# Performance work log

Measured on AMD Instinct MI355X. Metric: run time of the kernel, lower is better.

The kernel has to match this reference:

```python
import jax, jax.numpy as jnp
import numpy as np


def _mlp(x, w1, b1, w2, b2):
    # generic 2-layer MLP (stand-in for ConfiguredModule's combine_mlp / embedding_mlp)
    return jax.nn.gelu(x @ w1 + b1) @ w2 + b2


def setup_inputs() -> dict:
    key = jax.random.key(0)
    ks = jax.random.split(key, 8)
    B, N, A = 8, 128, 64          # molecules, atoms, nfeature
    Rr, Ra = 32, 16               # radial / angular geometry shifts
    P = N * (N - 1) // 2          # 8128 atom pairs
    d_pair, H, nembed = 32, 512, 256

    def rnd(k, shp, scale=1.0):
        return jax.random.normal(k, shp, dtype=jnp.float32) * scale

    return {
        "gr": rnd(ks[0], (B, N, Rr, N), 0.1),
        "ga": rnd(ks[1], (B, N, Ra, P), 0.1),
        "afv": rnd(ks[2], (B, N, A)),
        # combine_mlp: 2A -> 2A -> d_pair
        "cw1": rnd(ks[3], (2 * A, 2 * A), 1.0 / np.sqrt(2 * A)),
        "cb1": jnp.zeros((2 * A,), jnp.float32),
        "cw2": rnd(ks[4], (2 * A, d_pair), 1.0 / np.sqrt(2 * A)),
        "cb2": jnp.zeros((d_pair,), jnp.float32),
        # embedding_mlp: Rr*A + Ra*d_pair -> H -> nembed
        "ew1": rnd(ks[5], (Rr * A + Ra * d_pair, H), 1.0 / np.sqrt(Rr * A + Ra * d_pair)),
        "eb1": jnp.zeros((H,), jnp.float32),
        "ew2": rnd(ks[6], (H, nembed), 1.0 / np.sqrt(H)),
        "eb2": jnp.zeros((nembed,), jnp.float32),
    }


def reference(gr, ga, afv, cw1, cb1, cw2, cb2, ew1, eb1, ew2, eb2):
    B, N, A = afv.shape
    # _combine_afv_1: pairwise outer sum/product, upper-triangular (i<j) pairs.
    # Instead of materializing [B, 2A, N, N] and masking, gather pairs directly
    # (row-major i<j order matches torch's triu boolean-mask indexing).
    ii, jj = jnp.triu_indices(N, k=1)           # [P]
    ai = afv[:, ii, :]                           # [B, P, A]
    aj = afv[:, jj, :]                           # [B, P, A]
    afv_pair = jnp.concatenate([ai + aj, ai * aj], axis=-1)  # [B, P, 2A]
    afv_pair = _mlp(afv_pair, cw1, cb1, cw2, cb2)            # [B, P, d_pair]

    # grv = matmul(gr, afv[:, None]) : [B, N, Rr, N] @ [B, 1, N, A] -> [B, N, Rr, A]
    grv = jnp.einsum('bnrm,bma->bnra', gr, afv).reshape(B, N, -1)
    # gav = matmul(ga, afv_pair[:, None]) : [B, N, Ra, P] @ [B, 1, P, d] -> [B, N, Ra, d]
    gav = jnp.einsum('bnap,bpd->bnad', ga, afv_pair).reshape(B, N, -1)

    aef = _mlp(jnp.concatenate([grv, gav], axis=-1), ew1, eb1, ew2, eb2)  # [B, N, nembed]
    return aef, afv
```

## Files before the change

### kernel.cpp

```cpp
#include <hip/hip_runtime.h>
#include <math.h>

#define BB 8
#define NN 128
#define AA 64
#define RR 32
#define RA 16
#define PP 8128
#define DP 32
#define HH 512
#define EE 256
#define XDIM 2560

static constexpr size_t WS_PAIRT = 0;
static constexpr size_t WS_XB    = WS_PAIRT + (size_t)BB*DP*PP/2;
static constexpr size_t WS_EW1B  = WS_XB + (size_t)BB*NN*XDIM/2;
static constexpr size_t WS_CW1T  = WS_EW1B + (size_t)HH*XDIM/2;
static constexpr size_t WS_CW2T  = WS_CW1T + (size_t)128*128/2;
static constexpr size_t WS_EW2B  = WS_CW2T + (size_t)DP*128/2;
static constexpr size_t WS_HB    = WS_EW2B + (size_t)EE*HH/2;

typedef __attribute__((ext_vector_type(8))) short bf16x8;
typedef __attribute__((ext_vector_type(4))) float f32x4;

__device__ __forceinline__ float gelu_f(float x) {
    float u = 0.7978845608028654f * (x + 0.044715f * x * x * x);
    float au = fabsf(u);
    float e = __expf(-2.0f * au);
    float th = (1.0f - e) / (1.0f + e);
    th = copysignf(th, u);
    return 0.5f * x * (1.0f + th);
}

__device__ __forceinline__ unsigned short f2bf(float x) {
    union { float f; unsigned u; } v; v.f = x;
    unsigned r = v.u + 0x7fffu + ((v.u >> 16) & 1u);
    return (unsigned short)(r >> 16);
}

__device__ __forceinline__ bf16x8 pack_bf16x8(float4 a, float4 b) {
    bf16x8 r;
    r[0] = (short)f2bf(a.x); r[1] = (short)f2bf(a.y);
    r[2] = (short)f2bf(a.z); r[3] = (short)f2bf(a.w);
    r[4] = (short)f2bf(b.x); r[5] = (short)f2bf(b.y);
    r[6] = (short)f2bf(b.z); r[7] = (short)f2bf(b.w);
    return r;
}

__global__ __launch_bounds__(256) void prep_k(
    const float* __restrict__ cw1, const float* __restrict__ cw2,
    unsigned short* __restrict__ cw1T, unsigned short* __restrict__ cw2T)
{
    const int bid = blockIdx.x, t = threadIdx.x;
    if (bid < 16) {
        int idx = bid * 256 + t;
        int n = idx >> 5;
        int k0 = (idx & 31) * 4;
        ushort4 o;
        o.x = f2bf(cw1[(size_t)(k0 + 0) * 128 + n]);
        o.y = f2bf(cw1[(size_t)(k0 + 1) * 128 + n]);
        o.z = f2bf(cw1[(size_t)(k0 + 2) * 128 + n]);
        o.w = f2bf(cw1[(size_t)(k0 + 3) * 128 + n]);
        *(ushort4*)(cw1T + (size_t)n * 128 + k0) = o;
    } else {
        int idx = (bid - 16) * 256 + t;
        int d = idx >> 5;
        int k0 = (idx & 31) * 4;
        ushort4 o;
        o.x = f2bf(cw2[(size_t)(k0 + 0) * DP + d]);
        o.y = f2bf(cw2[(size_t)(k0 + 1) * DP + d]);
        o.z = f2bf(cw2[(size_t)(k0 + 2) * DP + d]);
        o.w = f2bf(cw2[(size_t)(k0 + 3) * DP + d]);
        *(ushort4*)(cw2T + (size_t)d * 128 + k0) = o;
    }
}

__global__ __launch_bounds__(256) void stage1_k(
    const float* __restrict__ afv, const unsigned short* __restrict__ cw1T,
    const float* __restrict__ cb1, const unsigned short* __restrict__ cw2T,
    const float* __restrict__ cb2, unsigned short* __restrict__ pairT)
{
    __shared__ unsigned short sm[16384];
    __shared__ int iis[64], jjs[64];
    const int bid = blockIdx.x;
    const int t = threadIdx.x;
    const int w = t >> 6, lane = t & 63;
    const int lm = lane & 15, lg = lane >> 4;

    const int b = bid / 127;
    const int pbase = (bid % 127) * 64;
    unsigned short* X = sm;
    unsigned short* Hs = sm + 8192;

    if (t < 64) {
        int p = pbase + t;
        int i = 0;
        while (i < 126) {
            int nx = i + 1;
            int off = nx * 127 - (nx * (nx - 1)) / 2;
            if (off <= p) i = nx; else break;
        }
        int off = i * 127 - (i * (i - 1)) / 2;
        iis[t] = i;
        jjs[t] = i + 1 + (p - off);
    }
    __syncthreads();
    {
        int pp = t & 63, seg = t >> 6;
        const float* ar = afv + (size_t)(b * NN + iis[pp]) * AA + seg * 16;
        const float* br = afv + (size_t)(b * NN + jjs[pp]) * AA + seg * 16;
        float4 xa = *(const float4*)(ar),     xb2 = *(const float4*)(ar + 4);
        float4 xc = *(const float4*)(ar + 8), xd = *(const float4*)(ar + 12);
        float4 ya = *(const float4*)(br),     yb = *(const float4*)(br + 4);
        float4 yc = *(const float4*)(br + 8), yd = *(const float4*)(br + 12);
        float4 s0 = make_float4(xa.x + ya.x, xa.y + ya.y, xa.z + ya.z, xa.w + ya.w);
        float4 s1 = make_float4(xb2.x + yb.x, xb2.y + yb.y, xb2.z + yb.z, xb2.w + yb.w);
        float4 s2 = make_float4(xc.x + yc.x, xc.y + yc.y, xc.z + yc.z, xc.w + yc.w);
        float4 s3 = make_float4(xd.x + yd.x, xd.y + yd.y, xd.z + yd.z, xd.w + yd.w);
        float4 p0 = make_float4(xa.x * ya.x, xa.y * ya.y, xa.z * ya.z, xa.w * ya.w);
        float4 p1 = make_float4(xb2.x * yb.x, xb2.y * yb.y, xb2.z * yb.z, xb2.w * yb.w);
        float4 p2 = make_float4(xc.x * yc.x, xc.y * yc.y, xc.z * yc.z, xc.w * yc.w);
        float4 p3 = make_float4(xd.x * yd.x, xd.y * yd.y, xd.z * yd.z, xd.w * yd.w);
        int gs = seg * 2, gp = 8 + seg * 2, sw = pp & 7;
        *(bf16x8*)(X + pp * 128 + (((gs + 0) ^ sw) * 8)) = pack_bf16x8(s0, s1);
        *(bf16x8*)(X + pp * 128 + (((gs + 1) ^ sw) * 8)) = pack_bf16x8(s2, s3);
        *(bf16x8*)(X + pp * 128 + (((gp + 0) ^ sw) * 8)) = pack_bf16x8(p0, p1);
        *(bf16x8*)(X + pp * 128 + (((gp + 1) ^ sw) * 8)) = pack_bf16x8(p2, p3);
    }
    __syncthreads();
    const int wn = w * 32;
    f32x4 acc1[4][2];
    #pragma unroll
    for (int i = 0; i < 4; ++i)
        #pragma unroll
        for (int j = 0; j < 2; ++j) acc1[i][j] = 0.f;
    #pragma unroll
    for (int ks = 0; ks < 4; ++ks) {
        int g = ks * 4 + lg;
        bf16x8 a[4];
        #pragma unroll
        for (int mi = 0; mi < 4; ++mi) {
            int row = mi * 16 + lm;
            a[mi] = *(const bf16x8*)(X + row * 128 + ((g ^ (row & 7)) * 8));
        }
        #pragma unroll
        for (int ni = 0; ni < 2; ++ni) {
            bf16x8 bv = *(const bf16x8*)(cw1T + (size_t)(wn + ni * 16 + lm) * 128 +
                                         ks * 32 + lg * 8);
            #pragma unroll
            for (int mi = 0; mi < 4; ++mi)
                acc1[mi][ni] = __builtin_amdgcn_mfma_f32_16x16x32_bf16(
                    a[mi], bv, acc1[mi][ni], 0, 0, 0);
        }
    }
    #pragma unroll
    for (int ni = 0; ni < 2; ++ni) {
        int n = wn + ni * 16 + lm;
        float bb = cb1[n];
        int gn = n >> 3, ne = n & 7;
        #pragma unroll
        for (int mi = 0; mi < 4; ++mi)
            #pragma unroll
            for (int r = 0; r < 4; ++r) {
                int row = mi * 16 + lg * 4 + r;
                Hs[row * 128 + ((gn ^ (row & 7)) * 8 + ne)] =
                    f2bf(gelu_f(acc1[mi][ni][r] + bb));
            }
    }
    __syncthreads();
    f32x4 acc2[2];
    acc2[0] = 0.f; acc2[1] = 0.f;
    #pragma unroll
    for (int ks = 0; ks < 4; ++ks) {
        int row = w * 16 + lm;
        int g = ks * 4 + lg;
        bf16x8 a2 = *(const bf16x8*)(Hs + row * 128 + ((g ^ (row & 7)) * 8));
        #pragma unroll
        for (int ni = 0; ni < 2; ++ni) {
            bf16x8 bv = *(const bf16x8*)(cw2T + (size_t)(ni * 16 + lm) * 128 +
                                         ks * 32 + lg * 8);
            acc2[ni] = __builtin_amdgcn_mfma_f32_16x16x32_bf16(a2, bv, acc2[ni], 0, 0, 0);
        }
    }
    {
        unsigned short* T = sm;
        __syncthreads();
        #pragma unroll
        for (int ni = 0; ni < 2; ++ni) {
            int d = ni * 16 + lm;
            float bb = cb2[d];
            #pragma unroll
            for (int r = 0; r < 4; ++r) {
                int p = w * 16 + lg * 4 + r;
                T[d * 64 + p] = f2bf(acc2[ni][r] + bb);
            }
        }
        __syncthreads();
        int d = t >> 3, slot = t & 7;
        bf16x8 v = *(const bf16x8*)(T + d * 64 + slot * 8);
        *(bf16x8*)(pairT + ((size_t)b * DP + d) * PP + pbase + slot * 8) = v;
    }
}

__global__ __launch_bounds__(256) void gav_k(
    const float* __restrict__ ga, const unsigned short* __restrict__ pairT,
    unsigned short* __restrict__ Xb,
    const float* __restrict__ gr, const float* __restrict__ afv,
    const float* __restrict__ ew1, unsigned short* __restrict__ ew1bT,
    const float* __restrict__ ew2, unsigned short* __restrict__ ew2bT,
    float* __restrict__ out2)
{
    __shared__ unsigned short sm[24576];
    const int bid = blockIdx.x;
    const int t = threadIdx.x;
    const int w = t >> 6, lane = t & 63;
    const int lm = lane & 15, lg = lane >> 4;

    if (bid >= 2176) {
        int idx = (bid - 2176) * 256 + t;
        float4 v = *(const float4*)(afv + (size_t)idx * 4);
        *(float4*)(out2 + (size_t)idx * 4) = v;
        return;
    }
    if (bid >= 2048) {
        int q = (bid - 2048) * 256 + t;
        int n = q & 255;
        int k0 = (q >> 8) * 4;
        ushort4 o;
        o.x = f2bf(ew2[(size_t)(k0 + 0) * EE + n]);
        o.y = f2bf(ew2[(size_t)(k0 + 1) * EE + n]);
        o.z = f2bf(ew2[(size_t)(k0 + 2) * EE + n]);
        o.w = f2bf(ew2[(size_t)(k0 + 3) * EE + n]);
        *(ushort4*)(ew2bT + (size_t)n * HH + k0) = o;
        return;
    }
    if (bid >= 768) {
        int q = (bid - 768) * 256 + t;
        int n = q & 511;
        int k0 = (q >> 9) * 4;
        ushort4 o;
        o.x = f2bf(ew1[(size_t)(k0 + 0) * HH + n]);
        o.y = f2bf(ew1[(size_t)(k0 + 1) * HH + n]);
        o.z = f2bf(ew1[(size_t)(k0 + 2) * HH + n]);
        o.w = f2bf(ew1[(size_t)(k0 + 3) * HH + n]);
        *(ushort4*)(ew1bT + (size_t)n * XDIM + k0) = o;
        return;
    }

    if (bid >= 512) {
        const int gb = bid - 512;
        const int b = gb >> 5;
        const int rbase = (gb & 31) * 128;
        const float* gab = gr + ((size_t)b * 4096 + rbase) * NN;
        unsigned short* As  = sm;
        unsigned short* Bs2 = sm + 16384;
        {
            const int srow = t >> 1, half = t & 1;
            const float* arow = gab + (size_t)srow * NN + half * 64;
            #pragma unroll
            for (int q = 0; q < 8; ++q) {
                float4 x0 = *(const float4*)(arow + q * 8);
                float4 x1 = *(const float4*)(arow + q * 8 + 4);
                bf16x8 v = pack_bf16x8(x0, x1);
                int g = half * 8 + q;
                *(bf16x8*)(As + srow * 128 + ((g ^ (srow & 7)) * 8)) = v;
            }
        }
        #pragma unroll
        for (int q = 0; q < 8; ++q) {
            int pos = t + q * 256;
            int m = pos >> 4, f4i = pos & 15;
            float4 v = *(const float4*)(afv + (size_t)(b * NN + m) * AA + f4i * 4);
            int gm = m >> 3, me = m & 7;
            float vv[4] = {v.x, v.y, v.z, v.w};
            #pragma unroll
            for (int i = 0; i < 4; ++i) {
                int a = f4i * 4 + i;
                Bs2[a * 128 + ((gm ^ (a & 7)) * 8 + me)] = f2bf(vv[i]);
            }
        }
        __syncthreads();
        const int wm = w * 32;
        f32x4 acc[2][4];
        #pragma unroll
        for (int i = 0; i < 2; ++i)
            #pragma unroll
            for (int j = 0; j < 4; ++j) acc[i][j] = 0.f;
        #pragma unroll
        for (int ks = 0; ks < 4; ++ks) {
            int g = ks * 4 + lg;
            int r0 = wm + lm, r1 = wm + 16 + lm;
            bf16x8 a0 = *(const bf16x8*)(As + r0 * 128 + ((g ^ (r0 & 7)) * 8));
            bf16x8 a1 = *(const bf16x8*)(As + r1 * 128 + ((g ^ (r1 & 7)) * 8));
            #pragma unroll
            for (int ni = 0; ni < 4; ++ni) {
                int a = ni * 16 + lm;
                bf16x8 bv = *(const bf16x8*)(Bs2 + a * 128 + ((g ^ (a & 7)) * 8));
                acc[0][ni] = __builtin_amdgcn_mfma_f32_16x16x32_bf16(a0, bv, acc[0][ni], 0, 0, 0);
                acc[1][ni] = __builtin_amdgcn_mfma_f32_16x16x32_bf16(a1, bv, acc[1][ni], 0, 0, 0);
            }
        }
        __syncthreads();
        unsigned short* T = sm;
        #pragma unroll
        for (int mi = 0; mi < 2; ++mi)
            #pragma unroll
            for (int ni = 0; ni < 4; ++ni)
                #pragma unroll
                for (int r = 0; r < 4; ++r)
                    T[(wm + mi * 16 + lg * 4 + r) * 64 + ni * 16 + lm] =
                        f2bf(acc[mi][ni][r]);
        __syncthreads();
        #pragma unroll
        for (int q = 0; q < 4; ++q) {
            int idx = t + q * 256;
            int rr2 = idx >> 3, slot = idx & 7;
            bf16x8 v = *(const bf16x8*)(T + rr2 * 64 + slot * 8);
            int grow = rbase + rr2;
            *(bf16x8*)(Xb + ((size_t)(b * NN) + (grow >> 5)) * XDIM +
                       (grow & 31) * 64 + slot * 8) = v;
        }
        return;
    }

    const int b = bid & 7, rt = bid >> 3;
    const int rbase = rt * 32;
    const int srow = t >> 3, slot = t & 7;
    const int wr = (w & 1) * 16, wc = (w >> 1) * 16;
    unsigned short* As = sm;
    unsigned short* Bs = sm + 4096;

    f32x4 acc = 0.f;

    const float* gab = ga + (size_t)(b * 2048 + rbase) * PP;
    const unsigned short* pbT = pairT + (size_t)b * DP * PP;

    float4 ra[4];
    bf16x8 rb0, rb1;
    {
        int k0 = slot * 8;
        ra[0] = *(const float4*)(gab + (size_t)srow * PP + k0);
        ra[1] = *(const float4*)(gab + (size_t)srow * PP + k0 + 4);
        ra[2] = *(const float4*)(gab + (size_t)srow * PP + k0 + 64);
        ra[3] = *(const float4*)(gab + (size_t)srow * PP + k0 + 68);
        rb0 = *(const bf16x8*)(pbT + (size_t)srow * PP + k0);
        rb1 = *(const bf16x8*)(pbT + (size_t)srow * PP + k0 + 64);
    }

    for (int it = 0; it < 64; ++it) {
        __syncthreads();
        const int sw = srow & 7;
        const int g0 = (slot ^ sw) * 8;
        const int g1 = ((slot ^ sw) + 8) * 8;
        *(bf16x8*)(As + srow * 128 + g0) = pack_bf16x8(ra[0], ra[1]);
        *(bf16x8*)(As + srow * 128 + g1) = pack_bf16x8(ra[2], ra[3]);
        *(bf16x8*)(Bs + srow * 128 + g0) = rb0;
        *(bf16x8*)(Bs + srow * 128 + g1) = rb1;
        __syncthreads();
        if (it + 1 < 64) {
            int kn = (it + 1) * 128 + slot * 8;
            int k1 = kn + 64; if (k1 > PP - 8) k1 = PP - 8;
            ra[0] = *(const float4*)(gab + (size_t)srow * PP + kn);
            ra[1] = *(const float4*)(gab + (size_t)srow * PP + kn + 4);
            ra[2] = *(const float4*)(gab + (size_t)srow * PP + k1);
            ra[3] = *(const float4*)(gab + (size_t)srow * PP + k1 + 4);
            rb0 = *(const bf16x8*)(pbT + (size_t)srow * PP + kn);
            rb1 = *(const bf16x8*)(pbT + (size_t)srow * PP + k1);
        }
        if (it < 63) {
            #pragma unroll
            for (int ks = 0; ks < 4; ++ks) {
                int gg = ks * 4 + lg;
                int rowa = wr + lm;
                int rowb = wc + lm;
                bf16x8 a  = *(const bf16x8*)(As + rowa * 128 + ((gg ^ (rowa & 7)) * 8));
                bf16x8 bv = *(const bf16x8*)(Bs + rowb * 128 + ((gg ^ (rowb & 7)) * 8));
                acc = __builtin_amdgcn_mfma_f32_16x16x32_bf16(a, bv, acc, 0, 0, 0);
            }
        } else {
            #pragma unroll
            for (int ks = 0; ks < 2; ++ks) {
                int gg = ks * 4 + lg;
                int rowa = wr + lm;
                int rowb = wc + lm;
                bf16x8 a  = *(const bf16x8*)(As + rowa * 128 + ((gg ^ (rowa & 7)) * 8));
                bf16x8 bv = *(const bf16x8*)(Bs + rowb * 128 + ((gg ^ (rowb & 7)) * 8));
                acc = __builtin_amdgcn_mfma_f32_16x16x32_bf16(a, bv, acc, 0, 0, 0);
            }
        }
    }
    #pragma unroll
    for (int r = 0; r < 4; ++r) {
        int grow = rbase + wr + lg * 4 + r;
        int n = grow >> 4, a2 = grow & 15;
        int d = wc + lm;
        Xb[(size_t)(b * NN + n) * XDIM + 2048 + a2 * DP + d] = f2bf(acc[r]);
    }
}

__global__ __launch_bounds__(256) void mlp1_k(
    const unsigned short* __restrict__ Xb,
    const unsigned short* __restrict__ Wt,
    const float* __restrict__ eb1, unsigned short* __restrict__ Hb)
{
    __shared__ unsigned short As[32 * 64];
    __shared__ unsigned short Bs[32 * 64];
    const int bid = blockIdx.x;
    const int ct = bid & 15, rt = bid >> 4;
    const int rbase = rt * 32, nbase = ct * 32;
    const int t = threadIdx.x;
    const int w = t >> 6, lane = t & 63;
    const int lm = lane & 15, lg = lane >> 4;
    const int wr = (w & 1) * 16, wc = (w >> 1) * 16;
    const int srow = t >> 3, sg = t & 7;

    f32x4 acc = 0.f;

    const unsigned short* Arow = Xb + (size_t)(rbase + srow) * XDIM;
    const unsigned short* Brow = Wt + (size_t)(nbase + srow) * XDIM;

    bf16x8 rA = *(const bf16x8*)(Arow + sg * 8);
    bf16x8 rB = *(const bf16x8*)(Brow + sg * 8);

    for (int it = 0; it < 40; ++it) {
        __syncthreads();
        const int sw = srow & 7;
        *(bf16x8*)(As + srow * 64 + ((sg ^ sw) * 8)) = rA;
        *(bf16x8*)(Bs + srow * 64 + ((sg ^ sw) * 8)) = rB;
        __syncthreads();
        if (it + 1 < 40) {
            int kn = (it + 1) * 64;
            rA = *(const bf16x8*)(Arow + kn + sg * 8);
            rB = *(const bf16x8*)(Brow + kn + sg * 8);
        }
        #pragma unroll
        for (int ks = 0; ks < 2; ++ks) {
            int g = ks * 4 + lg;
            int r0 = wr + lm, r1 = wc + lm;
            bf16x8 a  = *(const bf16x8*)(As + r0 * 64 + ((g ^ (r0 & 7)) * 8));
            bf16x8 bv = *(const bf16x8*)(Bs + r1 * 64 + ((g ^ (r1 & 7)) * 8));
            acc = __builtin_amdgcn_mfma_f32_16x16x32_bf16(a, bv, acc, 0, 0, 0);
        }
    }
    const int col = nbase + wc + lm;
    const float bb = eb1[col];
    #pragma unroll
    for (int r = 0; r < 4; ++r) {
        int row = rbase + wr + lg * 4 + r;
        Hb[(size_t)row * HH + col] = f2bf(gelu_f(acc[r] + bb));
    }
}

__global__ __launch_bounds__(256) void mlp2_k(
    const unsigned short* __restrict__ Hb,
    const unsigned short* __restrict__ Wt,
    const float* __restrict__ eb2, float* __restrict__ out)
{
    __shared__ unsigned short As[32 * 64];
    __shared__ unsigned short Bs[32 * 64];
    const int bid = blockIdx.x;
    const int ct = bid & 7, rt = bid >> 3;
    const int rbase = rt * 32, nbase = ct * 32;
    const int t = threadIdx.x;
    const int w = t >> 6, lane = t & 63;
    const int lm = lane & 15, lg = lane >> 4;
    const int wr = (w & 1) * 16, wc = (w >> 1) * 16;
    const int srow = t >> 3, sg = t & 7;

    f32x4 acc = 0.f;

    const unsigned short* Arow = Hb + (size_t)(rbase + srow) * HH;
    const unsigned short* Brow = Wt + (size_t)(nbase + srow) * HH;

    bf16x8 rA = *(const bf16x8*)(Arow + sg * 8);
    bf16x8 rB = *(const bf16x8*)(Brow + sg * 8);

    for (int it = 0; it < 8; ++it) {
        __syncthreads();
        const int sw = srow & 7;
        *(bf16x8*)(As + srow * 64 + ((sg ^ sw) * 8)) = rA;
        *(bf16x8*)(Bs + srow * 64 + ((sg ^ sw) * 8)) = rB;
        __syncthreads();
        if (it + 1 < 8) {
            int kn = (it + 1) * 64;
            rA = *(const bf16x8*)(Arow + kn + sg * 8);
            rB = *(const bf16x8*)(Brow + kn + sg * 8);
        }
        #pragma unroll
        for (int ks = 0; ks < 2; ++ks) {
            int g = ks * 4 + lg;
            int r0 = wr + lm, r1 = wc + lm;
            bf16x8 a  = *(const bf16x8*)(As + r0 * 64 + ((g ^ (r0 & 7)) * 8));
            bf16x8 bv = *(const bf16x8*)(Bs + r1 * 64 + ((g ^ (r1 & 7)) * 8));
            acc = __builtin_amdgcn_mfma_f32_16x16x32_bf16(a, bv, acc, 0, 0, 0);
        }
    }
    const int col = nbase + wc + lm;
    const float bb = eb2[col];
    #pragma unroll
    for (int r = 0; r < 4; ++r) {
        int row = rbase + wr + lg * 4 + r;
        out[(size_t)row * EE + col] = acc[r] + bb;
    }
}

extern "C" void kernel_launch(void* const* d_in, const int* in_sizes, int n_in,
                              void* d_out, int out_size, void* d_ws, size_t ws_size,
                              hipStream_t stream) {
    const float* gr  = (const float*)d_in[0];
    const float* ga  = (const float*)d_in[1];
    const float* afv = (const float*)d_in[2];
    const float* cw1 = (const float*)d_in[3];
    const float* cb1 = (const float*)d_in[4];
    const float* cw2 = (const float*)d_in[5];
    const float* cb2 = (const float*)d_in[6];
    const float* ew1 = (const float*)d_in[7];
    const float* eb1 = (const float*)d_in[8];
    const float* ew2 = (const float*)d_in[9];
    const float* eb2 = (const float*)d_in[10];
    float* out = (float*)d_out;
    float* ws = (float*)d_ws;

    unsigned short* pairT  = (unsigned short*)(ws + WS_PAIRT);
    unsigned short* Xb     = (unsigned short*)(ws + WS_XB);
    unsigned short* ew1bT  = (unsigned short*)(ws + WS_EW1B);
    unsigned short* cw1T   = (unsigned short*)(ws + WS_CW1T);
    unsigned short* cw2T   = (unsigned short*)(ws + WS_CW2T);
    unsigned short* ew2bT  = (unsigned short*)(ws + WS_EW2B);
    unsigned short* Hb     = (unsigned short*)(ws + WS_HB);

    prep_k<<<dim3(20), dim3(256), 0, stream>>>(cw1, cw2, cw1T, cw2T);
    stage1_k<<<dim3(1016), dim3(256), 0, stream>>>(afv, cw1T, cb1, cw2T, cb2, pairT);
    gav_k<<<dim3(2240), dim3(256), 0, stream>>>(ga, pairT, Xb, gr, afv,
                                                ew1, ew1bT, ew2, ew2bT,
                                                out + (size_t)BB * NN * EE);
    mlp1_k<<<dim3(512), dim3(256), 0, stream>>>(Xb, ew1bT, eb1, Hb);
    mlp2_k<<<dim3(256), dim3(256), 0, stream>>>(Hb, ew2bT, eb2, out);
}
```

Baseline: 180.7 us.

## Double-buffer LDS tiles in GEMM kernels and remap blocks across XCDs

```diff
diff --git a/kernel.cpp b/kernel.cpp
--- a/kernel.cpp
+++ b/kernel.cpp
@@ -327,8 +327,6 @@
     const int rbase = rt * 32;
     const int srow = t >> 3, slot = t & 7;
     const int wr = (w & 1) * 16, wc = (w >> 1) * 16;
-    unsigned short* As = sm;
-    unsigned short* Bs = sm + 4096;
 
     f32x4 acc = 0.f;
 
@@ -337,44 +335,51 @@
 
     float4 ra[4];
     bf16x8 rb0, rb1;
-    {
-        int k0 = slot * 8;
-        ra[0] = *(const float4*)(gab + (size_t)srow * PP + k0);
-        ra[1] = *(const float4*)(gab + (size_t)srow * PP + k0 + 4);
-        ra[2] = *(const float4*)(gab + (size_t)srow * PP + k0 + 64);
-        ra[3] = *(const float4*)(gab + (size_t)srow * PP + k0 + 68);
-        rb0 = *(const bf16x8*)(pbT + (size_t)srow * PP + k0);
-        rb1 = *(const bf16x8*)(pbT + (size_t)srow * PP + k0 + 64);
-    }
+
+#define GAV_LOAD(IT)                                                         \
+    {                                                                        \
+        int kn = (IT) * 128 + slot * 8;                                      \
+        int k1 = kn + 64; if (k1 > PP - 8) k1 = PP - 8;                      \
+        ra[0] = *(const float4*)(gab + (size_t)srow * PP + kn);              \
+        ra[1] = *(const float4*)(gab + (size_t)srow * PP + kn + 4);          \
+        ra[2] = *(const float4*)(gab + (size_t)srow * PP + k1);              \
+        ra[3] = *(const float4*)(gab + (size_t)srow * PP + k1 + 4);          \
+        rb0 = *(const bf16x8*)(pbT + (size_t)srow * PP + kn);                \
+        rb1 = *(const bf16x8*)(pbT + (size_t)srow * PP + k1);                \
+    }
+
+#define GAV_WRITE(BUF)                                                      \
+    {                                                                        \
+        unsigned short* A_ = sm + (BUF) * 8192;                              \
+        unsigned short* B_ = A_ + 4096;                                      \
+        const int sw_ = srow & 7;                                            \
+        const int g0_ = (slot ^ sw_) * 8;                                    \
+        const int g1_ = ((slot ^ sw_) + 8) * 8;                              \
+        *(bf16x8*)(A_ + srow * 128 + g0_) = pack_bf16x8(ra[0], ra[1]);       \
+        *(bf16x8*)(A_ + srow * 128 + g1_) = pack_bf16x8(ra[2], ra[3]);       \
+        *(bf16x8*)(B_ + srow * 128 + g0_) = rb0;                             \
+        *(bf16x8*)(B_ + srow * 128 + g1_) = rb1;                             \
+    }
+
+    GAV_LOAD(0);
+    GAV_WRITE(0);
+    __syncthreads();
+    GAV_LOAD(1);
 
     for (int it = 0; it < 64; ++it) {
-        __syncthreads();
-        const int sw = srow & 7;
-        const int g0 = (slot ^ sw) * 8;
-        const int g1 = ((slot ^ sw) + 8) * 8;
-        *(bf16x8*)(As + srow * 128 + g0) = pack_bf16x8(ra[0], ra[1]);
-        *(bf16x8*)(As + srow * 128 + g1) = pack_bf16x8(ra[2], ra[3]);
-        *(bf16x8*)(Bs + srow * 128 + g0) = rb0;
-        *(bf16x8*)(Bs + srow * 128 + g1) = rb1;
-        __syncthreads();
-        if (it + 1 < 64) {
-            int kn = (it + 1) * 128 + slot * 8;
-            int k1 = kn + 64; if (k1 > PP - 8) k1 = PP - 8;
-            ra[0] = *(const float4*)(gab + (size_t)srow * PP + kn);
-            ra[1] = *(const float4*)(gab + (size_t)srow * PP + kn + 4);
-            ra[2] = *(const float4*)(gab + (size_t)srow * PP + k1);
-            ra[3] = *(const float4*)(gab + (size_t)srow * PP + k1 + 4);
-            rb0 = *(const bf16x8*)(pbT + (size_t)srow * PP + kn);
-            rb1 = *(const bf16x8*)(pbT + (size_t)srow * PP + k1);
-        }
+        const int cur = it & 1;
+        const unsigned short* Ac = sm + cur * 8192;
+        const unsigned short* Bc = Ac + 4096;
+        if (it + 1 < 64) GAV_WRITE(cur ^ 1);
+        if (it + 2 < 64) GAV_LOAD(it + 2);
         if (it < 63) {
             #pragma unroll
             for (int ks = 0; ks < 4; ++ks) {
                 int gg = ks * 4 + lg;
                 int rowa = wr + lm;
                 int rowb = wc + lm;
-                bf16x8 a  = *(const bf16x8*)(As + rowa * 128 + ((gg ^ (rowa & 7)) * 8));
-                bf16x8 bv = *(const bf16x8*)(Bs + rowb * 128 + ((gg ^ (rowb & 7)) * 8));
+                bf16x8 a  = *(const bf16x8*)(Ac + rowa * 128 + ((gg ^ (rowa & 7)) * 8));
+                bf16x8 bv = *(const bf16x8*)(Bc + rowb * 128 + ((gg ^ (rowb & 7)) * 8));
                 acc = __builtin_amdgcn_mfma_f32_16x16x32_bf16(a, bv, acc, 0, 0, 0);
             }
         } else {
@@ -383,11 +388,12 @@
                 int gg = ks * 4 + lg;
                 int rowa = wr + lm;
                 int rowb = wc + lm;
-                bf16x8 a  = *(const bf16x8*)(As + rowa * 128 + ((gg ^ (rowa & 7)) * 8));
-                bf16x8 bv = *(const bf16x8*)(Bs + rowb * 128 + ((gg ^ (rowb & 7)) * 8));
+                bf16x8 a  = *(const bf16x8*)(Ac + rowa * 128 + ((gg ^ (rowa & 7)) * 8));
+                bf16x8 bv = *(const bf16x8*)(Bc + rowb * 128 + ((gg ^ (rowb & 7)) * 8));
                 acc = __builtin_amdgcn_mfma_f32_16x16x32_bf16(a, bv, acc, 0, 0, 0);
             }
         }
+        __syncthreads();
     }
     #pragma unroll
     for (int r = 0; r < 4; ++r) {
@@ -403,10 +409,11 @@
     const unsigned short* __restrict__ Wt,
     const float* __restrict__ eb1, unsigned short* __restrict__ Hb)
 {
-    __shared__ unsigned short As[32 * 64];
-    __shared__ unsigned short Bs[32 * 64];
+    __shared__ unsigned short sm[8192];
     const int bid = blockIdx.x;
-    const int ct = bid & 15, rt = bid >> 4;
+    const int xcd = bid & 7, idx = bid >> 3;
+    const int rt = (xcd << 2) | (idx & 3);
+    const int ct = idx >> 2;
     const int rbase = rt * 32, nbase = ct * 32;
     const int t = threadIdx.x;
     const int w = t >> 6, lane = t & 63;
@@ -419,28 +426,35 @@
     const unsigned short* Arow = Xb + (size_t)(rbase + srow) * XDIM;
     const unsigned short* Brow = Wt + (size_t)(nbase + srow) * XDIM;
 
-    bf16x8 rA = *(const bf16x8*)(Arow + sg * 8);
-    bf16x8 rB = *(const bf16x8*)(Brow + sg * 8);
+    bf16x8 rA, rB;
+
+#define M1_LOAD(IT)  { rA = *(const bf16x8*)(Arow + (IT) * 64 + sg * 8);     \
+                       rB = *(const bf16x8*)(Brow + (IT) * 64 + sg * 8); }
+#define M1_WRITE(BUF) { unsigned short* A_ = sm + (BUF) * 4096;              \
+                        unsigned short* B_ = A_ + 2048;                      \
+                        const int sw_ = srow & 7;                            \
+                        *(bf16x8*)(A_ + srow * 64 + ((sg ^ sw_) * 8)) = rA;  \
+                        *(bf16x8*)(B_ + srow * 64 + ((sg ^ sw_) * 8)) = rB; }
+
+    M1_LOAD(0); M1_WRITE(0);
+    __syncthreads();
+    M1_LOAD(1);
 
     for (int it = 0; it < 40; ++it) {
-        __syncthreads();
-        const int sw = srow & 7;
-        *(bf16x8*)(As + srow * 64 + ((sg ^ sw) * 8)) = rA;
-        *(bf16x8*)(Bs + srow * 64 + ((sg ^ sw) * 8)) = rB;
-        __syncthreads();
-        if (it + 1 < 40) {
-            int kn = (it + 1) * 64;
-            rA = *(const bf16x8*)(Arow + kn + sg * 8);
-            rB = *(const bf16x8*)(Brow + kn + sg * 8);
-        }
+        const int cur = it & 1;
+        const unsigned short* Ac = sm + cur * 4096;
+        const unsigned short* Bc = Ac + 2048;
+        if (it + 1 < 40) M1_WRITE(cur ^ 1);
+        if (it + 2 < 40) M1_LOAD(it + 2);
         #pragma unroll
         for (int ks = 0; ks < 2; ++ks) {
             int g = ks * 4 + lg;
             int r0 = wr + lm, r1 = wc + lm;
-            bf16x8 a  = *(const bf16x8*)(As + r0 * 64 + ((g ^ (r0 & 7)) * 8));
-            bf16x8 bv = *(const bf16x8*)(Bs + r1 * 64 + ((g ^ (r1 & 7)) * 8));
+            bf16x8 a  = *(const bf16x8*)(Ac + r0 * 64 + ((g ^ (r0 & 7)) * 8));
+            bf16x8 bv = *(const bf16x8*)(Bc + r1 * 64 + ((g ^ (r1 & 7)) * 8));
             acc = __builtin_amdgcn_mfma_f32_16x16x32_bf16(a, bv, acc, 0, 0, 0);
         }
+        __syncthreads();
     }
     const int col = nbase + wc + lm;
     const float bb = eb1[col];
@@ -456,10 +470,11 @@
     const unsigned short* __restrict__ Wt,
     const float* __restrict__ eb2, float* __restrict__ out)
 {
-    __shared__ unsigned short As[32 * 64];
-    __shared__ unsigned short Bs[32 * 64];
+    __shared__ unsigned short sm[8192];
     const int bid = blockIdx.x;
-    const int ct = bid & 7, rt = bid >> 3;
+    const int xcd = bid & 7, idx = bid >> 3;
+    const int rt = (xcd << 2) | (idx & 3);
+    const int ct = idx >> 2;
     const int rbase = rt * 32, nbase = ct * 32;
     const int t = threadIdx.x;
     const int w = t >> 6, lane = t & 63;
@@ -472,28 +487,35 @@
     const unsigned short* Arow = Hb + (size_t)(rbase + srow) * HH;
     const unsigned short* Brow = Wt + (size_t)(nbase + srow) * HH;
 
-    bf16x8 rA = *(const bf16x8*)(Arow + sg * 8);
-    bf16x8 rB = *(const bf16x8*)(Brow + sg * 8);
+    bf16x8 rA, rB;
+
+#define M2_LOAD(IT)  { rA = *(const bf16x8*)(Arow + (IT) * 64 + sg * 8);     \
+                       rB = *(const bf16x8*)(Brow + (IT) * 64 + sg * 8); }
+#define M2_WRITE(BUF) { unsigned short* A_ = sm + (BUF) * 4096;              \
+                        unsigned short* B_ = A_ + 2048;                      \
+                        const int sw_ = srow & 7;                            \
+                        *(bf16x8*)(A_ + srow * 64 + ((sg ^ sw_) * 8)) = rA;  \
+                        *(bf16x8*)(B_ + srow * 64 + ((sg ^ sw_) * 8)) = rB; }
+
+    M2_LOAD(0); M2_WRITE(0);
+    __syncthreads();
+    M2_LOAD(1);
 
     for (int it = 0; it < 8; ++it) {
-        __syncthreads();
-        const int sw = srow & 7;
-        *(bf16x8*)(As + srow * 64 + ((sg ^ sw) * 8)) = rA;
-        *(bf16x8*)(Bs + srow * 64 + ((sg ^ sw) * 8)) = rB;
-        __syncthreads();
-        if (it + 1 < 8) {
-            int kn = (it + 1) * 64;
-            rA = *(const bf16x8*)(Arow + kn + sg * 8);
-            rB = *(const bf16x8*)(Brow + kn + sg * 8);
-        }
+        const int cur = it & 1;
+        const unsigned short* Ac = sm + cur * 4096;
+        const unsigned short* Bc = Ac + 2048;
+        if (it + 1 < 8) M2_WRITE(cur ^ 1);
+        if (it + 2 < 8) M2_LOAD(it + 2);
         #pragma unroll
         for (int ks = 0; ks < 2; ++ks) {
             int g = ks * 4 + lg;
             int r0 = wr + lm, r1 = wc + lm;
-            bf16x8 a  = *(const bf16x8*)(As + r0 * 64 + ((g ^ (r0 & 7)) * 8));
-            bf16x8 bv = *(const bf16x8*)(Bs + r1 * 64 + ((g ^ (r1 & 7)) * 8));
+            bf16x8 a  = *(const bf16x8*)(Ac + r0 * 64 + ((g ^ (r0 & 7)) * 8));
+            bf16x8 bv = *(const bf16x8*)(Bc + r1 * 64 + ((g ^ (r1 & 7)) * 8));
             acc = __builtin_amdgcn_mfma_f32_16x16x32_bf16(a, bv, acc, 0, 0, 0);
         }
+        __syncthreads();
     }
     const int col = nbase + wc + lm;
     const float bb = eb2[col];
```

Result: faster. 171.0 us (-5.4%).
